# Kernel tuning notes

Measured on AMD Instinct MI355X. Metric: run time of the kernel, lower is better.

Reference implementation:

```python
import jax, jax.numpy as jnp
import numpy as np

B, S, F = 4, 4096, 1024
H, DK, R = 16, 64, 32  # n_head, d_k, low_rank; n_attn = H*DK = 1024


def _l2norm(x, eps=1e-12):
    # torch.nn.functional.normalize(p=2, dim=-1)
    n = jnp.sqrt(jnp.sum(x * x, axis=-1, keepdims=True))
    return x / jnp.maximum(n, eps)


def setup_inputs() -> dict:
    key = jax.random.key(0)
    ks = jax.random.split(key, 16)
    s = 0.02
    inp = {
        "query": jax.random.normal(ks[0], (B, S, F), jnp.float32),
        "key": jax.random.normal(ks[1], (B, S, F), jnp.float32),
        "value": jax.random.normal(ks[2], (B, S, F), jnp.float32),
        "p_layer": 1,
        # linear_q / linear_k (linear_v unused in p_layer branch but kept for fidelity)
        "Wq": jax.random.normal(ks[3], (H * DK, F), jnp.float32) * s,
        "bq": jnp.zeros((H * DK,), jnp.float32),
        "Wk": jax.random.normal(ks[4], (H * DK, F), jnp.float32) * s,
        "bk": jnp.zeros((H * DK,), jnp.float32),
        "Wv": jax.random.normal(ks[5], (H * DK, F), jnp.float32) * s,
        "bv": jnp.zeros((H * DK,), jnp.float32),
        # low-rank projections (orthogonal-init stand-ins)
        "We": jax.random.normal(ks[6], (H, DK, R), jnp.float32) * s,
        "Wr": jax.random.normal(ks[7], (H, DK, R), jnp.float32) * s,
        "Lam": jax.random.uniform(ks[8], (H, R), jnp.float32),
        # concate_weight: Linear(2R -> DK)
        "Wc": jax.random.normal(ks[9], (DK, 2 * R), jnp.float32) * s,
        "bc": jnp.zeros((DK,), jnp.float32),
        # linear_out: Linear(H*DK -> F)
        "Wo": jax.random.normal(ks[10], (F, H * DK), jnp.float32) * s,
        "bo": jnp.zeros((F,), jnp.float32),
    }
    return inp


def reference(query, key, value, Wq, bq, Wk, bk, Wv, bv, We, Wr, Lam, Wc, bc, Wo, bo, p_layer):
    n_batch, seq_len, _ = query.shape
    # projections -> (B, H, S, DK)
    q = (query @ Wq.T + bq).reshape(n_batch, seq_len, H, DK).transpose(0, 2, 1, 3)
    k = (key @ Wk.T + bk).reshape(n_batch, seq_len, H, DK).transpose(0, 2, 1, 3)
    if p_layer:  # static Python int
        normal = jnp.arange(1, seq_len + 1, dtype=q.dtype)[None, None, :, None]
        q = jnp.cumsum(q, axis=2) / normal  # causal running average
        k = jnp.cumsum(k, axis=2) / normal
        q = _l2norm(q)
        k = _l2norm(k)
        escore = jnp.einsum('bhnd,hde->bhne', q, We)  # (B,H,S,R)
        rscore = jnp.einsum('bhnd,hde->bhne', k, Wr)
        scores = jnp.concatenate((escore, rscore), axis=-1)  # (B,H,S,2R)
        x = scores @ Wc.T + bc  # (B,H,S,DK)
        x = x.transpose(0, 2, 1, 3).reshape(n_batch, seq_len, H * DK)
    else:
        v = (value @ Wv.T + bv).reshape(n_batch, seq_len, H, DK).transpose(0, 2, 1, 3)
        att = jax.nn.softmax(jnp.einsum('bhqd,bhkd->bhqk', q, k) / jnp.sqrt(jnp.asarray(DK, q.dtype)), axis=-1)
        x = jnp.einsum('bhqk,bhkd->bhqd', att, v).transpose(0, 2, 1, 3).reshape(n_batch, seq_len, H * DK)
    return x @ Wo.T + bo
```

## Files before the change

### kernel.cpp

```cpp
#include <hip/hip_runtime.h>

typedef __bf16 bf16x8 __attribute__((ext_vector_type(8)));
typedef float floatx4 __attribute__((ext_vector_type(4)));

__device__ __forceinline__ unsigned short f2bf(float x) {
  union { float f; unsigned u; } v; v.f = x;
  unsigned u = v.u;
  unsigned r = (u + 0x7FFFu + ((u >> 16) & 1u)) >> 16;
  return (unsigned short)r;
}
__device__ __forceinline__ float bf2f(unsigned short x) {
  union { unsigned u; float f; } v; v.u = ((unsigned)x) << 16;
  return v.f;
}
__device__ __forceinline__ float fast_rcp(float x) {
#if defined(__has_builtin) && __has_builtin(__builtin_amdgcn_rcpf)
  return __builtin_amdgcn_rcpf(x);
#else
  return 1.0f / x;
#endif
}
__device__ __forceinline__ float fast_rsq(float x) {
#if defined(__has_builtin) && __has_builtin(__builtin_amdgcn_rsqf)
  return __builtin_amdgcn_rsqf(x);
#else
  return 1.0f / sqrtf(x);
#endif
}

__device__ __forceinline__ void stage16(const unsigned short* __restrict__ g,
                                        unsigned short* s, int lane) {
#if defined(__has_builtin) && __has_builtin(__builtin_amdgcn_global_load_lds)
  __builtin_amdgcn_global_load_lds((const __attribute__((address_space(1))) void*)g,
                                   (__attribute__((address_space(3))) void*)s,
                                   16, 0, 0);
#else
  *(uint4*)(s + (size_t)lane * 8) = *(const uint4*)g;
#endif
}

__global__ void cvt_bf16(const float* __restrict__ in, unsigned short* __restrict__ out, int n4) {
  int i = blockIdx.x * 256 + threadIdx.x;
  if (i >= n4) return;
  const float4 v = ((const float4*)in)[i];
  ushort4 o;
  o.x = f2bf(v.x); o.y = f2bf(v.y); o.z = f2bf(v.z); o.w = f2bf(v.w);
  ((ushort4*)out)[i] = o;
}

#define LDSE (256 * 64)
#define BAR() __builtin_amdgcn_s_barrier()

#define RD_A(b, mh) {                                                          \
  _Pragma("unroll") for (int ii = 0; ii < 4; ++ii) {                           \
    _Pragma("unroll") for (int s = 0; s < 2; ++s) {                            \
      af[ii][s] = *(const bf16x8*)(rA + (b) * LDSE +                           \
                                   ((mh) * 128 + ii * 16) * 64 +               \
                                   (((s << 2) | quad) ^ key) * 8);             \
    } } }

#define RD_B(b, nh, dst) {                                                     \
  _Pragma("unroll") for (int jj = 0; jj < 2; ++jj) {                           \
    _Pragma("unroll") for (int s = 0; s < 2; ++s) {                            \
      dst[jj][s] = *(const bf16x8*)(rB + (b) * LDSE +                          \
                                    ((nh) * 128 + jj * 16) * 64 +              \
                                    (((s << 2) | quad) ^ key) * 8);            \
    } } }

#define STAGE_A(b, mh, t) {                                                    \
  stage16(gA + (size_t)((mh) * 128) * K + (size_t)(t) * 64,                    \
          sAw + (b) * LDSE + ((mh) * 128) * 64, lane);                         \
  stage16(gA + (size_t)((mh) * 128 + 8) * K + (size_t)(t) * 64,                \
          sAw + (b) * LDSE + ((mh) * 128 + 8) * 64, lane); }

#define STAGE_B(b, nh, t) {                                                    \
  stage16(gB + (size_t)((nh) * 128) * K + (size_t)(t) * 64,                    \
          sBw + (b) * LDSE + ((nh) * 128) * 64, lane);                         \
  stage16(gB + (size_t)((nh) * 128 + 8) * K + (size_t)(t) * 64,                \
          sBw + (b) * LDSE + ((nh) * 128 + 8) * 64, lane); }

#define MFMA_PH(mh, nh, bfx) {                                                 \
  __builtin_amdgcn_s_setprio(1);                                               \
  _Pragma("unroll") for (int s = 0; s < 2; ++s) {                              \
    _Pragma("unroll") for (int ii = 0; ii < 4; ++ii) {                         \
      _Pragma("unroll") for (int jj = 0; jj < 2; ++jj) {                       \
        acc[mh][nh][ii][jj] = __builtin_amdgcn_mfma_f32_16x16x32_bf16(         \
            af[ii][s], bfx[jj][s], acc[mh][nh][ii][jj], 0, 0, 0);              \
      } } }                                                                    \
  __builtin_amdgcn_s_setprio(0); }

#define TILE5(b, t, S, Y) {                                                    \
  if (S) { STAGE_A((b) ^ 1, 0, (t) + 1); STAGE_B((b) ^ 1, 0, (t) + 1);         \
           STAGE_B((b) ^ 1, 1, (t) + 1); STAGE_A((b) ^ 1, 1, (t) + 1); }       \
  RD_B(b, 0, bf0); RD_A(b, 0);                                                 \
  MFMA_PH(0, 0, bf0);                                                          \
  RD_B(b, 1, bf1);                                                             \
  MFMA_PH(0, 1, bf1);                                                          \
  RD_A(b, 1);                                                                  \
  MFMA_PH(1, 1, bf1);                                                          \
  MFMA_PH(1, 0, bf0);                                                          \
  if (Y) { asm volatile("s_waitcnt vmcnt(0)" ::: "memory"); BAR(); } }

template <int OUT_BF16>
__global__ __launch_bounds__(512, 2) void gemm8p(const unsigned short* __restrict__ A,
                                                 const unsigned short* __restrict__ B,
                                                 const unsigned short* __restrict__ B2,
                                                 const float* __restrict__ bias,
                                                 const float* __restrict__ bias2,
                                                 void* __restrict__ Cv,
                                                 int M, int N, int K, int halfM) {
  __shared__ unsigned short As[2 * 256 * 64];
  __shared__ unsigned short Bs[2 * 256 * 64];
  const int tid = threadIdx.x;
  const int w = tid >> 6;
  const int lane = tid & 63;

  const int NT = N >> 8;
  const int id = blockIdx.x;
  const int x = id & 7;
  const int g = id >> 3;
  const int nt_ = g % NT;
  const int mt = x + 8 * (g / NT);
  const int bm = mt * 256, bn = nt_ * 256;

  const unsigned short* Bp = (bm >= halfM) ? B2 : B;
  const float* biasp = (bm >= halfM) ? bias2 : bias;

  const int row16 = lane & 15, quad = lane >> 4, key = lane & 7;
  const int l8 = lane >> 3, lk = lane & 7;
  const int swz = (lk ^ l8) * 8;

  const unsigned short* gA = A + (size_t)(bm + 16 * w + l8) * K + swz;
  const unsigned short* gB = Bp + (size_t)(bn + 16 * w + l8) * K + swz;
  unsigned short* sAw = As + (16 * w) * 64;
  unsigned short* sBw = Bs + (16 * w) * 64;

  const unsigned short* rA = As + ((w >> 2) * 64 + row16) * 64;
  const unsigned short* rB = Bs + ((w & 3) * 32 + row16) * 64;

  floatx4 acc[2][2][4][2] = {};
  bf16x8 af[4][2], bf0[2][2], bf1[2][2];

  STAGE_A(0, 0, 0); STAGE_B(0, 0, 0); STAGE_B(0, 1, 0); STAGE_A(0, 1, 0);
  asm volatile("s_waitcnt vmcnt(0)" ::: "memory");
  BAR();

  const int npair = K >> 7;
  for (int it = 0; it < npair - 1; ++it) {
    TILE5(0, 2 * it, true, true);
    TILE5(1, 2 * it + 1, true, true);
  }
  TILE5(0, 2 * npair - 2, true, true);
  TILE5(1, 2 * npair - 1, false, false);

#pragma unroll
  for (int nh = 0; nh < 2; ++nh)
#pragma unroll
    for (int jj = 0; jj < 2; ++jj) {
      const int gcol = bn + nh * 128 + (w & 3) * 32 + jj * 16 + row16;
      const float bb = biasp ? biasp[gcol] : 0.0f;
#pragma unroll
      for (int mh = 0; mh < 2; ++mh)
#pragma unroll
        for (int ii = 0; ii < 4; ++ii) {
          const int grow = bm + mh * 128 + (w >> 2) * 64 + ii * 16 + quad * 4;
#pragma unroll
          for (int r = 0; r < 4; ++r) {
            float v = acc[mh][nh][ii][jj][r] + bb;
            if (OUT_BF16)
              ((unsigned short*)Cv)[(size_t)(grow + r) * N + gcol] = f2bf(v);
            else
              ((float*)Cv)[(size_t)(grow + r) * N + gcol] = v;
          }
        }
    }
}

__global__ void scan_partial(const unsigned short* __restrict__ proj, float* __restrict__ partial) {
  const int t = blockIdx.x, chunk = blockIdx.y, b = blockIdx.z;
  const int c4 = threadIdx.x * 4;
  const unsigned short* p =
      proj + ((size_t)t * 4 + b) * 4096 * 1024 + (size_t)chunk * 64 * 1024 + c4;
  float4 s = {0.f, 0.f, 0.f, 0.f};
  for (int i = 0; i < 64; i++) {
    const ushort4 v = *(const ushort4*)(p + (size_t)i * 1024);
    s.x += bf2f(v.x); s.y += bf2f(v.y); s.z += bf2f(v.z); s.w += bf2f(v.w);
  }
  *(float4*)(partial + ((size_t)(t * 4 + b) * 64 + chunk) * 1024 + c4) = s;
}

__global__ void scan_apply(const unsigned short* __restrict__ proj,
                           const float* __restrict__ partial,
                           unsigned short* __restrict__ qkn) {
  const int t = blockIdx.x, chunk = blockIdx.y, b = blockIdx.z;
  const int c4 = threadIdx.x * 4;
  const float* pp = partial + (size_t)(t * 4 + b) * 64 * 1024 + c4;
  float4 run = {0.f, 0.f, 0.f, 0.f};
  for (int j = 0; j < chunk; j++) {
    const float4 v = *(const float4*)(pp + (size_t)j * 1024);
    run.x += v.x; run.y += v.y; run.z += v.z; run.w += v.w;
  }
  const unsigned short* p =
      proj + ((size_t)t * 4 + b) * 4096 * 1024 + (size_t)chunk * 64 * 1024 + c4;
  unsigned short* o = qkn + (size_t)b * 4096 * 2048 + (size_t)chunk * 64 * 2048 + t * 1024 + c4;
  for (int i = 0; i < 64; i++) {
    const ushort4 v = *(const ushort4*)(p + (size_t)i * 1024);
    run.x += bf2f(v.x); run.y += bf2f(v.y); run.z += bf2f(v.z); run.w += bf2f(v.w);
    const int s = chunk * 64 + i;
    const float inv = fast_rcp((float)(s + 1));
    const float a0 = run.x * inv, a1 = run.y * inv, a2 = run.z * inv, a3 = run.w * inv;
    float sq = a0 * a0 + a1 * a1 + a2 * a2 + a3 * a3;
    sq += __shfl_xor(sq, 8);
    sq += __shfl_xor(sq, 4);
    sq += __shfl_xor(sq, 2);
    sq += __shfl_xor(sq, 1);
    const float sc = fast_rsq(fmaxf(sq, 1e-24f));
    ushort4 ov;
    ov.x = f2bf(a0 * sc); ov.y = f2bf(a1 * sc); ov.z = f2bf(a2 * sc); ov.w = f2bf(a3 * sc);
    *(ushort4*)(o + (size_t)i * 2048) = ov;
  }
}

__global__ void make_A(const float* __restrict__ We, const float* __restrict__ Wr,
                       const float* __restrict__ Wc, float* __restrict__ Asm) {
  const int t = blockIdx.x >> 4, h = blockIdx.x & 15;
  const float* W = (t ? Wr : We) + (size_t)h * 64 * 32;
  for (int e = threadIdx.x; e < 4096; e += 256) {
    const int d = e >> 6, dk = e & 63;
    float s = 0.f;
    for (int r = 0; r < 32; r++) s += W[d * 32 + r] * Wc[dk * 64 + t * 32 + r];
    Asm[(size_t)blockIdx.x * 4096 + e] = s;
  }
}

__global__ __launch_bounds__(256) void make_G(const float* __restrict__ Asm,
                                              const float* __restrict__ Wo,
                                              unsigned short* __restrict__ Gt) {
  __shared__ float At[64 * 65];
  __shared__ float WoSh[64 * 64];
  const int th = blockIdx.x, t = th >> 4, h = th & 15;
  const int f0 = blockIdx.y * 64;
  const int tid = threadIdx.x;
  for (int e = tid; e < 4096; e += 256) {
    const int d = e >> 6, dk = e & 63;
    At[dk * 65 + d] = Asm[(size_t)th * 4096 + e];
  }
  for (int e = tid; e < 4096; e += 256) {
    const int fl = e >> 6, dk = e & 63;
    WoSh[e] = Wo[(size_t)(f0 + fl) * 1024 + h * 64 + dk];
  }
  __syncthreads();
  const int d = tid & 63;
  const int fsub = tid >> 6;
#pragma unroll 4
  for (int it = 0; it < 16; ++it) {
    const int fl = it * 4 + fsub;
    float s = 0.f;
#pragma unroll
    for (int dk4 = 0; dk4 < 16; ++dk4) {
      const float4 wv = *(const float4*)&WoSh[fl * 64 + dk4 * 4];
      s += At[(dk4 * 4 + 0) * 65 + d] * wv.x + At[(dk4 * 4 + 1) * 65 + d] * wv.y +
           At[(dk4 * 4 + 2) * 65 + d] * wv.z + At[(dk4 * 4 + 3) * 65 + d] * wv.w;
    }
    Gt[(size_t)(f0 + fl) * 2048 + t * 1024 + h * 64 + d] = f2bf(s);
  }
}

__global__ void make_c0(const float* __restrict__ bc, const float* __restrict__ bo,
                        const float* __restrict__ Wo, float* __restrict__ c0) {
  const int f = blockIdx.x * 4 + (threadIdx.x >> 6);
  const int lane = threadIdx.x & 63;
  const float bcl = bc[lane];
  float s = 0.f;
  for (int j = lane; j < 1024; j += 64) s += bcl * Wo[(size_t)f * 1024 + j];
#pragma unroll
  for (int off = 32; off; off >>= 1) s += __shfl_xor(s, off);
  if (lane == 0) c0[f] = s + bo[f];
}

extern "C" void kernel_launch(void* const* d_in, const int* in_sizes, int n_in,
                              void* d_out, int out_size, void* d_ws, size_t ws_size,
                              hipStream_t stream) {
  const float* query = (const float*)d_in[0];
  const float* key_  = (const float*)d_in[1];
  const float* Wq = (const float*)d_in[4];
  const float* bq = (const float*)d_in[5];
  const float* Wk = (const float*)d_in[6];
  const float* bk = (const float*)d_in[7];
  const float* We = (const float*)d_in[10];
  const float* Wr = (const float*)d_in[11];
  const float* Wc = (const float*)d_in[13];
  const float* bc = (const float*)d_in[14];
  const float* Wo = (const float*)d_in[15];
  const float* bo = (const float*)d_in[16];

  char* ws = (char*)d_ws;
  unsigned short* qkbf = (unsigned short*)ws;
  unsigned short* Wbf  = (unsigned short*)(ws + 67108864);
  unsigned short* Gt   = (unsigned short*)(ws + 71303168);
  float* partial       = (float*)(ws + 71303168);
  float* Asm           = (float*)(ws + 75497472);
  float* c0            = (float*)(ws + 76021760);

  unsigned short* proj = (unsigned short*)d_out;

  cvt_bf16<<<16384, 256, 0, stream>>>(query, qkbf, 4194304);
  cvt_bf16<<<16384, 256, 0, stream>>>(key_, qkbf + 16777216, 4194304);
  cvt_bf16<<<1024, 256, 0, stream>>>(Wq, Wbf, 262144);
  cvt_bf16<<<1024, 256, 0, stream>>>(Wk, Wbf + 1048576, 262144);

  gemm8p<1><<<512, 512, 0, stream>>>(qkbf, Wbf, Wbf + 1048576, bq, bk, proj,
                                     32768, 1024, 1024, 16384);

  scan_partial<<<dim3(2, 64, 4), 256, 0, stream>>>(proj, partial);
  scan_apply<<<dim3(2, 64, 4), 256, 0, stream>>>(proj, partial, qkbf);

  make_A<<<32, 256, 0, stream>>>(We, Wr, Wc, Asm);
  make_G<<<dim3(32, 16), 256, 0, stream>>>(Asm, Wo, Gt);
  make_c0<<<256, 256, 0, stream>>>(bc, bo, Wo, c0);

  gemm8p<0><<<256, 512, 0, stream>>>(qkbf, Gt, Gt, c0, c0, (float*)d_out,
                                     16384, 1024, 2048, 16384 * 2);
}
```

Baseline: 446.9 us.

## Pre-pack B operand into MFMA fragment layout and switch to 32x32x16 MFMA

The weight matrices (Wq/Wk and the fused G matrix) are now written in a fragment-packed layout so each wave can load its B fragments straight from global memory into registers. This drops the B tile from LDS staging, halving shared-memory use and LDS traffic. The inner loop also moves from 16x16x32 to 32x32x16 MFMA, with new accumulator indexing and epilogue mapping. The cost is direct global loads of B that are not shared across waves and may stall if L2 latency is not hidden.

```diff
diff --git a/kernel.cpp b/kernel.cpp
--- a/kernel.cpp
+++ b/kernel.cpp
@@ -2,6 +2,7 @@
 
 typedef __bf16 bf16x8 __attribute__((ext_vector_type(8)));
 typedef float floatx4 __attribute__((ext_vector_type(4)));
+typedef float floatx16 __attribute__((ext_vector_type(16)));
 
 __device__ __forceinline__ unsigned short f2bf(float x) {
   union { float f; unsigned u; } v; v.f = x;
@@ -48,69 +49,62 @@
   ((ushort4*)out)[i] = o;
 }
 
-#define LDSE (256 * 64)
+__global__ void cvt_pack_w(const float* __restrict__ W, unsigned short* __restrict__ Bp) {
+  int i = blockIdx.x * 256 + threadIdx.x;
+  int n = i >> 8;
+  int k4 = (i & 255) * 4;
+  const float4 v = *(const float4*)(W + (size_t)n * 1024 + k4);
+  const int base = (((n >> 5) * 64 + (k4 >> 4)) * 64 + ((k4 >> 3) & 1) * 32 + (n & 31)) * 8 + (k4 & 7);
+  ushort4 o; o.x = f2bf(v.x); o.y = f2bf(v.y); o.z = f2bf(v.z); o.w = f2bf(v.w);
+  *(ushort4*)(Bp + base) = o;
+}
+
+#define LDSE2 (256 * 64)
 #define BAR() __builtin_amdgcn_s_barrier()
-
-#define RD_A(b, mh) {                                                          \
-  _Pragma("unroll") for (int ii = 0; ii < 4; ++ii) {                           \
-    _Pragma("unroll") for (int s = 0; s < 2; ++s) {                            \
-      af[ii][s] = *(const bf16x8*)(rA + (b) * LDSE +                           \
-                                   ((mh) * 128 + ii * 16) * 64 +               \
-                                   (((s << 2) | quad) ^ key) * 8);             \
-    } } }
-
-#define RD_B(b, nh, dst) {                                                     \
-  _Pragma("unroll") for (int jj = 0; jj < 2; ++jj) {                           \
-    _Pragma("unroll") for (int s = 0; s < 2; ++s) {                            \
-      dst[jj][s] = *(const bf16x8*)(rB + (b) * LDSE +                          \
-                                    ((nh) * 128 + jj * 16) * 64 +              \
-                                    (((s << 2) | quad) ^ key) * 8);            \
-    } } }
 
 #define STAGE_A(b, mh, t) {                                                    \
   stage16(gA + (size_t)((mh) * 128) * K + (size_t)(t) * 64,                    \
-          sAw + (b) * LDSE + ((mh) * 128) * 64, lane);                         \
+          sAw + (b) * LDSE2 + ((mh) * 128) * 64, lane);                        \
   stage16(gA + (size_t)((mh) * 128 + 8) * K + (size_t)(t) * 64,                \
-          sAw + (b) * LDSE + ((mh) * 128 + 8) * 64, lane); }
-
-#define STAGE_B(b, nh, t) {                                                    \
-  stage16(gB + (size_t)((nh) * 128) * K + (size_t)(t) * 64,                    \
-          sBw + (b) * LDSE + ((nh) * 128) * 64, lane);                         \
-  stage16(gB + (size_t)((nh) * 128 + 8) * K + (size_t)(t) * 64,                \
-          sBw + (b) * LDSE + ((nh) * 128 + 8) * 64, lane); }
-
-#define MFMA_PH(mh, nh, bfx) {                                                 \
+          sAw + (b) * LDSE2 + ((mh) * 128 + 8) * 64, lane); }
+
+#define LOAD_B(t) {                                                            \
+  _Pragma("unroll") for (int nb = 0; nb < 2; ++nb) {                           \
+    _Pragma("unroll") for (int ks = 0; ks < 4; ++ks) {                         \
+      bq[nb][ks] = *(const bf16x8*)(gBl +                                      \
+          ((size_t)(cb0 + nb) * KB + ((t) * 4 + ks)) * 512);                   \
+    } } }
+
+#define KSTEP(b, ks) {                                                         \
+  _Pragma("unroll") for (int mh = 0; mh < 2; ++mh) {                           \
+    _Pragma("unroll") for (int rb = 0; rb < 2; ++rb) {                         \
+      af[mh * 2 + rb] = *(const bf16x8*)(rA + (b) * LDSE2 +                    \
+          (mh * 128 + rb * 32) * 64 + ((((ks) * 2) | hi) ^ key) * 8);          \
+    } }                                                                        \
   __builtin_amdgcn_s_setprio(1);                                               \
-  _Pragma("unroll") for (int s = 0; s < 2; ++s) {                              \
-    _Pragma("unroll") for (int ii = 0; ii < 4; ++ii) {                         \
-      _Pragma("unroll") for (int jj = 0; jj < 2; ++jj) {                       \
-        acc[mh][nh][ii][jj] = __builtin_amdgcn_mfma_f32_16x16x32_bf16(         \
-            af[ii][s], bfx[jj][s], acc[mh][nh][ii][jj], 0, 0, 0);              \
+  _Pragma("unroll") for (int mh = 0; mh < 2; ++mh) {                           \
+    _Pragma("unroll") for (int rb = 0; rb < 2; ++rb) {                         \
+      _Pragma("unroll") for (int nb = 0; nb < 2; ++nb) {                       \
+        acc[mh][rb][nb] = __builtin_amdgcn_mfma_f32_32x32x16_bf16(             \
+            af[mh * 2 + rb], bq[nb][ks], acc[mh][rb][nb], 0, 0, 0);            \
       } } }                                                                    \
   __builtin_amdgcn_s_setprio(0); }
 
-#define TILE5(b, t, S, Y) {                                                    \
-  if (S) { STAGE_A((b) ^ 1, 0, (t) + 1); STAGE_B((b) ^ 1, 0, (t) + 1);         \
-           STAGE_B((b) ^ 1, 1, (t) + 1); STAGE_A((b) ^ 1, 1, (t) + 1); }       \
-  RD_B(b, 0, bf0); RD_A(b, 0);                                                 \
-  MFMA_PH(0, 0, bf0);                                                          \
-  RD_B(b, 1, bf1);                                                             \
-  MFMA_PH(0, 1, bf1);                                                          \
-  RD_A(b, 1);                                                                  \
-  MFMA_PH(1, 1, bf1);                                                          \
-  MFMA_PH(1, 0, bf0);                                                          \
+#define TILE6(b, t, S, Y) {                                                    \
+  LOAD_B(t);                                                                   \
+  if (S) { STAGE_A((b) ^ 1, 0, (t) + 1); STAGE_A((b) ^ 1, 1, (t) + 1); }       \
+  KSTEP(b, 0); KSTEP(b, 1); KSTEP(b, 2); KSTEP(b, 3);                          \
   if (Y) { asm volatile("s_waitcnt vmcnt(0)" ::: "memory"); BAR(); } }
 
 template <int OUT_BF16>
-__global__ __launch_bounds__(512, 2) void gemm8p(const unsigned short* __restrict__ A,
-                                                 const unsigned short* __restrict__ B,
-                                                 const unsigned short* __restrict__ B2,
+__global__ __launch_bounds__(512, 2) void gemm32(const unsigned short* __restrict__ A,
+                                                 const unsigned short* __restrict__ Bp,
+                                                 const unsigned short* __restrict__ Bp2,
                                                  const float* __restrict__ bias,
                                                  const float* __restrict__ bias2,
                                                  void* __restrict__ Cv,
                                                  int M, int N, int K, int halfM) {
-  __shared__ unsigned short As[2 * 256 * 64];
-  __shared__ unsigned short Bs[2 * 256 * 64];
+  __shared__ __align__(16) unsigned short As[2 * 256 * 64];
   const int tid = threadIdx.x;
   const int w = tid >> 6;
   const int lane = tid & 63;
@@ -123,57 +117,57 @@
   const int mt = x + 8 * (g / NT);
   const int bm = mt * 256, bn = nt_ * 256;
 
-  const unsigned short* Bp = (bm >= halfM) ? B2 : B;
+  const unsigned short* Bf = (bm >= halfM) ? Bp2 : Bp;
   const float* biasp = (bm >= halfM) ? bias2 : bias;
 
-  const int row16 = lane & 15, quad = lane >> 4, key = lane & 7;
-  const int l8 = lane >> 3, lk = lane & 7;
-  const int swz = (lk ^ l8) * 8;
+  const int key = lane & 7, hi = lane >> 5;
+  const int l8 = lane >> 3;
+  const int swz = ((lane & 7) ^ l8) * 8;
 
   const unsigned short* gA = A + (size_t)(bm + 16 * w + l8) * K + swz;
-  const unsigned short* gB = Bp + (size_t)(bn + 16 * w + l8) * K + swz;
   unsigned short* sAw = As + (16 * w) * 64;
-  unsigned short* sBw = Bs + (16 * w) * 64;
-
-  const unsigned short* rA = As + ((w >> 2) * 64 + row16) * 64;
-  const unsigned short* rB = Bs + ((w & 3) * 32 + row16) * 64;
-
-  floatx4 acc[2][2][4][2] = {};
-  bf16x8 af[4][2], bf0[2][2], bf1[2][2];
-
-  STAGE_A(0, 0, 0); STAGE_B(0, 0, 0); STAGE_B(0, 1, 0); STAGE_A(0, 1, 0);
+  const unsigned short* rA = As + ((w >> 2) * 64 + (lane & 31)) * 64;
+
+  const int KB = K >> 4;
+  const int cb0 = (bn >> 5) + (w & 3) * 2;
+  const unsigned short* gBl = Bf + (size_t)lane * 8;
+
+  floatx16 acc[2][2][2] = {};
+  bf16x8 af[4], bq[2][4];
+
+  STAGE_A(0, 0, 0); STAGE_A(0, 1, 0);
   asm volatile("s_waitcnt vmcnt(0)" ::: "memory");
   BAR();
 
-  const int npair = K >> 7;
-  for (int it = 0; it < npair - 1; ++it) {
-    TILE5(0, 2 * it, true, true);
-    TILE5(1, 2 * it + 1, true, true);
-  }
-  TILE5(0, 2 * npair - 2, true, true);
-  TILE5(1, 2 * npair - 1, false, false);
-
-#pragma unroll
-  for (int nh = 0; nh < 2; ++nh)
-#pragma unroll
-    for (int jj = 0; jj < 2; ++jj) {
-      const int gcol = bn + nh * 128 + (w & 3) * 32 + jj * 16 + row16;
-      const float bb = biasp ? biasp[gcol] : 0.0f;
-#pragma unroll
-      for (int mh = 0; mh < 2; ++mh)
-#pragma unroll
-        for (int ii = 0; ii < 4; ++ii) {
-          const int grow = bm + mh * 128 + (w >> 2) * 64 + ii * 16 + quad * 4;
-#pragma unroll
-          for (int r = 0; r < 4; ++r) {
-            float v = acc[mh][nh][ii][jj][r] + bb;
-            if (OUT_BF16)
-              ((unsigned short*)Cv)[(size_t)(grow + r) * N + gcol] = f2bf(v);
-            else
-              ((float*)Cv)[(size_t)(grow + r) * N + gcol] = v;
-          }
+  const int ntl = K >> 6;
+  for (int it = 0; it < (ntl >> 1) - 1; ++it) {
+    TILE6(0, 2 * it, true, true);
+    TILE6(1, 2 * it + 1, true, true);
+  }
+  TILE6(0, ntl - 2, true, true);
+  TILE6(1, ntl - 1, false, false);
+
+#pragma unroll
+  for (int nb = 0; nb < 2; ++nb) {
+    const int gcol = bn + (w & 3) * 64 + nb * 32 + (lane & 31);
+    const float bb = biasp ? biasp[gcol] : 0.0f;
+#pragma unroll
+    for (int mh = 0; mh < 2; ++mh) {
+#pragma unroll
+      for (int rb = 0; rb < 2; ++rb) {
+        const int rbase = bm + mh * 128 + (w >> 2) * 64 + rb * 32 + 4 * hi;
+#pragma unroll
+        for (int r = 0; r < 16; ++r) {
+          const int grow = rbase + (r & 3) + 8 * (r >> 2);
+          float v = acc[mh][rb][nb][r] + bb;
+          if (OUT_BF16)
+            ((unsigned short*)Cv)[(size_t)grow * N + gcol] = f2bf(v);
+          else
+            ((float*)Cv)[(size_t)grow * N + gcol] = v;
         }
+      }
     }
+  }
 }
 
 __global__ void scan_partial(const unsigned short* __restrict__ proj, float* __restrict__ partial) {
@@ -235,7 +229,7 @@
 
 __global__ __launch_bounds__(256) void make_G(const float* __restrict__ Asm,
                                               const float* __restrict__ Wo,
-                                              unsigned short* __restrict__ Gt) {
+                                              unsigned short* __restrict__ Gp) {
   __shared__ float At[64 * 65];
   __shared__ float WoSh[64 * 64];
   const int th = blockIdx.x, t = th >> 4, h = th & 15;
@@ -262,7 +256,9 @@
       s += At[(dk4 * 4 + 0) * 65 + d] * wv.x + At[(dk4 * 4 + 1) * 65 + d] * wv.y +
            At[(dk4 * 4 + 2) * 65 + d] * wv.z + At[(dk4 * 4 + 3) * 65 + d] * wv.w;
     }
-    Gt[(size_t)(f0 + fl) * 2048 + t * 1024 + h * 64 + d] = f2bf(s);
+    const int f = f0 + fl;
+    const int k = t * 1024 + h * 64 + d;
+    Gp[(((f >> 5) * 128 + (k >> 4)) * 64 + ((k >> 3) & 1) * 32 + (f & 31)) * 8 + (k & 7)] = f2bf(s);
   }
 }
 
@@ -297,7 +293,7 @@
   char* ws = (char*)d_ws;
   unsigned short* qkbf = (unsigned short*)ws;
   unsigned short* Wbf  = (unsigned short*)(ws + 67108864);
-  unsigned short* Gt   = (unsigned short*)(ws + 71303168);
+  unsigned short* Gp   = (unsigned short*)(ws + 71303168);
   float* partial       = (float*)(ws + 71303168);
   float* Asm           = (float*)(ws + 75497472);
   float* c0            = (float*)(ws + 76021760);
@@ -306,19 +302,19 @@
 
   cvt_bf16<<<16384, 256, 0, stream>>>(query, qkbf, 4194304);
   cvt_bf16<<<16384, 256, 0, stream>>>(key_, qkbf + 16777216, 4194304);
-  cvt_bf16<<<1024, 256, 0, stream>>>(Wq, Wbf, 262144);
-  cvt_bf16<<<1024, 256, 0, stream>>>(Wk, Wbf + 1048576, 262144);
-
-  gemm8p<1><<<512, 512, 0, stream>>>(qkbf, Wbf, Wbf + 1048576, bq, bk, proj,
+  cvt_pack_w<<<1024, 256, 0, stream>>>(Wq, Wbf);
+  cvt_pack_w<<<1024, 256, 0, stream>>>(Wk, Wbf + 1048576);
+
+  gemm32<1><<<512, 512, 0, stream>>>(qkbf, Wbf, Wbf + 1048576, bq, bk, proj,
                                      32768, 1024, 1024, 16384);
 
   scan_partial<<<dim3(2, 64, 4), 256, 0, stream>>>(proj, partial);
   scan_apply<<<dim3(2, 64, 4), 256, 0, stream>>>(proj, partial, qkbf);
 
   make_A<<<32, 256, 0, stream>>>(We, Wr, Wc, Asm);
-  make_G<<<dim3(32, 16), 256, 0, stream>>>(Asm, Wo, Gt);
+  make_G<<<dim3(32, 16), 256, 0, stream>>>(Asm, Wo, Gp);
   make_c0<<<256, 256, 0, stream>>>(bc, bo, Wo, c0);
 
-  gemm8p<0><<<256, 512, 0, stream>>>(qkbf, Gt, Gt, c0, c0, (float*)d_out,
+  gemm32<0><<<256, 512, 0, stream>>>(qkbf, Gp, Gp, c0, c0, (float*)d_out,
                                      16384, 1024, 2048, 16384 * 2);
 }
```

Measured after the change: 462.6 us. +3.5%, slower.
